# Performance work log

Measured on AMD Instinct MI355X. Metric: run time of the kernel, lower is better.

The kernel has to match this reference:

```python
import jax, jax.numpy as jnp
import numpy as np

TOKENS, IN_F, OUT_F = 8192, 4096, 4096
MAXQ = 15          # 4-bit
ZERO_POINT = 8     # (maxq + 1) // 2


def _make_24_mask(key, in_f, out_f):
    """Boolean 2:4 mask: exactly 2 True per contiguous group of 4 along in_f."""
    scores = jax.random.normal(key, (in_f // 4, 4, out_f), dtype=jnp.float32)
    # ascending sort along the group-of-4 axis; index 2 = 2nd largest value
    thresh = jnp.sort(scores, axis=1)[:, 2:3, :]
    mask = scores >= thresh  # keeps top-2 of each group of 4
    return mask.reshape(in_f, out_f)


def setup_inputs() -> dict:
    key = jax.random.key(0)
    k_x, k_q, k_m, k_s = jax.random.split(key, 4)
    x = jax.random.normal(k_x, (TOKENS, IN_F), dtype=jnp.float16)
    qvals = jax.random.randint(k_q, (IN_F, OUT_F), 0, MAXQ + 1, dtype=jnp.int32)
    mask = _make_24_mask(k_m, IN_F, OUT_F)
    # per-column scales (groupsize == infeatures -> one scale row)
    scales = (jax.random.uniform(k_s, (1, OUT_F), dtype=jnp.float32) * 0.01 + 0.001).astype(jnp.float16)
    return {"x": x, "qvals": qvals, "mask": mask, "scales": scales}


def reference(x, qvals, mask, scales):
    # Dequantize: W = (q - zero_point) * scale, then apply 2:4 sparsity mask.
    w = (qvals.astype(jnp.float32) - ZERO_POINT) * scales.astype(jnp.float32)  # [in, out]
    w = jnp.where(mask, w, 0.0).astype(x.dtype)
    # GEMM with fp32 accumulation (as the fused kernel does), output in x.dtype
    y = jnp.einsum("ti,io->to", x, w, preferred_element_type=jnp.float32)
    return y.astype(x.dtype)
```

## Files before the change

### kernel.cpp

```cpp
#include <hip/hip_runtime.h>
#include <stdint.h>

typedef short short8 __attribute__((ext_vector_type(8)));
typedef float floatx4 __attribute__((ext_vector_type(4)));

#define M_TOK 8192
#define K_IN  4096
#define N_OUT 4096
#define NT    (K_IN / 64)

static __device__ __forceinline__ float bf2f(ushort u) {
    union { uint32_t u; float f; } v;
    v.u = ((uint32_t)u) << 16;
    return v.f;
}
static __device__ __forceinline__ ushort f2bf(float f) {
    union { float f; uint32_t u; } v;
    v.f = f;
    uint32_t u = v.u;
    uint32_t r = (u + 0x7FFFu + ((u >> 16) & 1u)) >> 16;
    return (ushort)r;
}

__global__ void detect_zero_kernel(int* __restrict__ flags) {
    if (threadIdx.x < 3) flags[1 + threadIdx.x] = 0;
}

__global__ __launch_bounds__(256) void detect_count_kernel(
    const unsigned char* __restrict__ mb, int* __restrict__ flags) {
    const ushort* mh = (const ushort*)mb;
    const unsigned int* mw = (const unsigned int*)mb;
    __shared__ int sh[3];
    if (threadIdx.x < 3) sh[threadIdx.x] = 0;
    __syncthreads();
    int s = blockIdx.x * 256 + threadIdx.x;
    int grp = s & 255;
    int o   = (s * 97) & 4095;
    int c1 = 0, c2 = 0, c4 = 0;
    #pragma unroll
    for (int r = 0; r < 4; ++r) {
        size_t idx = (size_t)(4 * grp + r) * N_OUT + o;
        c1 += (mb[idx] != 0);
        c2 += (mh[idx] != 0);
        c4 += (mw[idx] != 0);
    }
    if (c1 != 2) atomicAdd(&sh[0], 1);
    if (c2 != 2) atomicAdd(&sh[1], 1);
    if (c4 != 2) atomicAdd(&sh[2], 1);
    __syncthreads();
    if (threadIdx.x == 0) {
        atomicAdd(&flags[1], sh[0]);
        atomicAdd(&flags[2], sh[1]);
        atomicAdd(&flags[3], sh[2]);
    }
}

__global__ void detect_final_kernel(int* __restrict__ flags) {
    if (threadIdx.x == 0) {
        int size = 4, best = flags[3];
        if (flags[2] < best) { size = 2; best = flags[2]; }
        if (flags[1] < best) { size = 1; }
        flags[0] = size;
    }
}

__global__ __launch_bounds__(256) void convert_x_kernel(
    const float* __restrict__ xf, ushort* __restrict__ Xb) {
    const int total = M_TOK * K_IN;
    const int stride = gridDim.x * 256 * 8;
    for (int i = (blockIdx.x * 256 + threadIdx.x) * 8; i < total; i += stride) {
        floatx4 f0 = *(const floatx4*)&xf[i];
        floatx4 f1 = *(const floatx4*)&xf[i + 4];
        short8 v;
        #pragma unroll
        for (int j = 0; j < 4; ++j) v[j]     = (short)f2bf(f0[j]);
        #pragma unroll
        for (int j = 0; j < 4; ++j) v[4 + j] = (short)f2bf(f1[j]);
        *(short8*)&Xb[i] = v;
    }
}

__global__ __launch_bounds__(256) void dequant_kernel(
    const int* __restrict__ q, const void* __restrict__ maskp,
    const float* __restrict__ scales, ushort* __restrict__ Bt,
    const int* __restrict__ flagp) {
    const int msize = flagp[0];
    const int i0 = blockIdx.x * 64;
    const int o0 = blockIdx.y * 64;
    const int tid = threadIdx.x;
    const unsigned char* mb = (const unsigned char*)maskp;
    const ushort* mh = (const ushort*)maskp;
    const unsigned int* mi = (const unsigned int*)maskp;
    __shared__ ushort T[64][72];

    for (int p = 0; p < 16; ++p) {
        int idx = p * 256 + tid;
        int r = idx >> 6, c = idx & 63;
        size_t gi = (size_t)(i0 + r) * N_OUT + (o0 + c);
        bool m;
        if (msize == 1)      m = (mb[gi] != 0);
        else if (msize == 2) m = (mh[gi] != 0);
        else                 m = (mi[gi] != 0);
        float s = scales[o0 + c];
        float w = m ? (float)(q[gi] - 8) * s : 0.0f;
        T[r][c] = f2bf(w);
    }
    __syncthreads();
    for (int p = 0; p < 2; ++p) {
        int ol = p * 32 + (tid >> 3);
        int i8 = (tid & 7) * 8;
        short8 v;
        #pragma unroll
        for (int j = 0; j < 8; ++j) v[j] = (short)T[i8 + j][ol];
        *(short8*)&Bt[(size_t)(o0 + ol) * K_IN + i0 + i8] = v;
    }
}

#define GL2L16(gp, lbase)                                                      \
    __builtin_amdgcn_global_load_lds(                                          \
        (const __attribute__((address_space(1))) void*)(gp),                   \
        (__attribute__((address_space(3))) void*)(lbase), 16, 0, 0)

__global__ __launch_bounds__(512, 2) void gemm_kernel(
    const ushort* __restrict__ X,
    const ushort* __restrict__ Bt,
    float* __restrict__ Y) {
    __shared__ ushort As[2][2][256][32];
    __shared__ ushort Bs[2][2][256][32];

    const int tid  = threadIdx.x;
    const int w    = tid >> 6;
    const int lane = tid & 63;

    const int r    = blockIdx.x >> 8;
    const int kb   = blockIdx.x & 255;
    const int xcd  = kb & 7;
    const int j    = kb >> 3;
    const int m_tile = r * 16 + (xcd & 1) * 8 + (j & 7);
    const int n_tile = (xcd >> 1) * 4 + (j >> 3);
    const int row0 = m_tile * 256;
    const int col0 = n_tile * 256;
    const int wm = w >> 2, wn = w & 3;

    floatx4 acc[8][4] = {};

    const int srow   = (w << 4) + (lane >> 2);
    const int schunk = (lane & 3) ^ ((lane >> 3) & 3);
    const ushort* gA = X  + (size_t)(row0 + srow) * K_IN + schunk * 8;
    const ushort* gB = Bt + (size_t)(col0 + srow) * K_IN + schunk * 8;

    const int fr = lane & 15, g = lane >> 4;
    const int fsw = (fr >> 1) & 3;

    #define STG(gbase, arr, bf, kh, tt)                                        \
        do {                                                                   \
            GL2L16(gbase + (size_t)(tt) * 64 + (kh) * 32,                      \
                   (char*)&arr[bf][kh][w * 16][0] + lane * 16);                \
            GL2L16(gbase + (size_t)128 * K_IN + (size_t)(tt) * 64 + (kh) * 32, \
                   (char*)&arr[bf][kh][128 + w * 16][0] + lane * 16);          \
        } while (0)

    #define PHASE(BF, KK, MH, READB, bfr, STAGE_STMT, GATE_STMT)               \
        do {                                                                   \
            if (READB) {                                                       \
                _Pragma("unroll")                                              \
                for (int n = 0; n < 4; ++n)                                    \
                    bfr[n] = *(const short8*)&Bs[BF][KK]                       \
                        [wn * 64 + n * 16 + fr][(g ^ fsw) * 8];                \
            }                                                                  \
            short8 afr[4];                                                     \
            _Pragma("unroll")                                                  \
            for (int m = 0; m < 4; ++m)                                        \
                afr[m] = *(const short8*)&As[BF][KK]                           \
                    [wm * 128 + (MH) * 64 + m * 16 + fr][(g ^ fsw) * 8];       \
            STAGE_STMT;                                                        \
            __builtin_amdgcn_s_barrier();                                      \
            asm volatile("s_waitcnt lgkmcnt(0)" ::: "memory");                 \
            __builtin_amdgcn_sched_barrier(0);                                 \
            __builtin_amdgcn_s_setprio(1);                                     \
            _Pragma("unroll")                                                  \
            for (int m = 0; m < 4; ++m)                                        \
                _Pragma("unroll")                                              \
                for (int n = 0; n < 4; ++n)                                    \
                    acc[(MH) * 4 + m][n] = __builtin_amdgcn_mfma_f32_16x16x32_bf16( \
                        afr[m], bfr[n], acc[(MH) * 4 + m][n], 0, 0, 0);        \
            __builtin_amdgcn_s_setprio(0);                                     \
            GATE_STMT;                                                         \
            __builtin_amdgcn_s_barrier();                                      \
        } while (0)

    #define GATE(c)                                                            \
        do {                                                                   \
            if (c) { asm volatile("s_waitcnt vmcnt(4)" ::: "memory"); }        \
            else   { asm volatile("s_waitcnt vmcnt(0)" ::: "memory"); }        \
        } while (0)

    STG(gA, As, 0, 0, 0);
    STG(gB, Bs, 0, 0, 0);
    STG(gA, As, 0, 1, 0);
    STG(gB, Bs, 0, 1, 0);
    STG(gA, As, 1, 0, 1);
    STG(gB, Bs, 1, 0, 1);
    asm volatile("s_waitcnt vmcnt(4)" ::: "memory");
    __builtin_amdgcn_s_barrier();

    short8 bfr0[4], bfr1[4];

    for (int i = 0; i < NT / 2; ++i) {
        const int t1 = 2 * i + 1, t2 = 2 * i + 2, t3 = 2 * i + 3;
        const bool s2 = (t2 < NT), s3 = (t3 < NT);

        PHASE(0, 0, 0, 1, bfr0, STG(gA, As, 1, 1, t1), );
        PHASE(0, 0, 1, 0, bfr0, STG(gB, Bs, 1, 1, t1), );
        PHASE(0, 1, 0, 1, bfr1, if (s2) STG(gA, As, 0, 0, t2), );
        PHASE(0, 1, 1, 0, bfr1, if (s2) STG(gB, Bs, 0, 0, t2), GATE(s2));

        PHASE(1, 0, 0, 1, bfr0, if (s2) STG(gA, As, 0, 1, t2), );
        PHASE(1, 0, 1, 0, bfr0, if (s2) STG(gB, Bs, 0, 1, t2), );
        PHASE(1, 1, 0, 1, bfr1, if (s3) STG(gA, As, 1, 0, t3), );
        PHASE(1, 1, 1, 0, bfr1, if (s3) STG(gB, Bs, 1, 0, t3), GATE(s3));
    }

    const int fq = lane >> 4;
    #pragma unroll
    for (int m = 0; m < 8; ++m)
        #pragma unroll
        for (int n = 0; n < 4; ++n)
            #pragma unroll
            for (int i = 0; i < 4; ++i) {
                int rr = row0 + wm * 128 + m * 16 + fq * 4 + i;
                int cc = col0 + wn * 64 + n * 16 + fr;
                Y[(size_t)rr * N_OUT + cc] = acc[m][n][i];
            }
    #undef GATE
    #undef PHASE
    #undef STG
}

__global__ __launch_bounds__(256) void fallback_kernel(
    const float* __restrict__ xf, const int* __restrict__ q,
    const void* __restrict__ maskp, const float* __restrict__ scales,
    float* __restrict__ Y, const int* __restrict__ flagp) {
    const int msize = flagp[0];
    const int o = blockIdx.x * 256 + threadIdx.x;
    const int t = blockIdx.y;
    const unsigned char* mb = (const unsigned char*)maskp;
    const ushort* mh = (const ushort*)maskp;
    const unsigned int* mi = (const unsigned int*)maskp;
    float s = scales[o];
    float acc = 0.f;
    for (int i = 0; i < K_IN; ++i) {
        float x = bf2f(f2bf(xf[(size_t)t * K_IN + i]));
        size_t gi = (size_t)i * N_OUT + o;
        bool m;
        if (msize == 1)      m = (mb[gi] != 0);
        else if (msize == 2) m = (mh[gi] != 0);
        else                 m = (mi[gi] != 0);
        if (m) acc += x * bf2f(f2bf((float)(q[gi] - 8) * s));
    }
    Y[(size_t)t * N_OUT + o] = acc;
}

extern "C" void kernel_launch(void* const* d_in, const int* in_sizes, int n_in,
                              void* d_out, int out_size, void* d_ws, size_t ws_size,
                              hipStream_t stream) {
    const float* x      = (const float*)d_in[0];
    const int*   q      = (const int*)d_in[1];
    const void*  mask   = d_in[2];
    const float* scales = (const float*)d_in[3];
    float* y = (float*)d_out;

    const size_t BT_OFF = 64;
    const size_t XB_OFF = BT_OFF + (size_t)N_OUT * K_IN * 2;
    const size_t need   = XB_OFF + (size_t)M_TOK * K_IN * 2;

    int* flags = (int*)d_ws;
    detect_zero_kernel<<<1, 64, 0, stream>>>(flags);
    detect_count_kernel<<<64, 256, 0, stream>>>(
        (const unsigned char*)mask, flags);
    detect_final_kernel<<<1, 64, 0, stream>>>(flags);

    if (ws_size >= need) {
        ushort* Bt = (ushort*)((char*)d_ws + BT_OFF);
        ushort* Xb = (ushort*)((char*)d_ws + XB_OFF);
        convert_x_kernel<<<4096, 256, 0, stream>>>(x, Xb);
        dequant_kernel<<<dim3(K_IN / 64, N_OUT / 64), 256, 0, stream>>>(
            q, mask, scales, Bt, flags);
        gemm_kernel<<<dim3((M_TOK / 256) * (N_OUT / 256)), 512, 0, stream>>>(
            Xb, Bt, y);
    } else {
        fallback_kernel<<<dim3(N_OUT / 256, M_TOK), 256, 0, stream>>>(
            x, q, mask, scales, y, flags);
    }
}
```

Before: 358.7 us.

## Restructure GEMM pipeline into 4-slot ring of 32-wide K tiles

Replaces the double-buffered 64-wide K staging (two 32-wide halves per buffer) with a 4-slot ring buffer of 32-wide K slices, prefetching three tiles ahead. Each K slice is split into two MFMA phases with the A and B loads for the slice three steps ahead interleaved between them. The LDS swizzle pattern also changes to match the new 32-column row layout. The aim is deeper load-ahead that better hides global latency. The cost is more barriers per unit of K and more outstanding loads, while LDS size stays the same.

```diff
diff --git a/kernel.cpp b/kernel.cpp
--- a/kernel.cpp
+++ b/kernel.cpp
@@ -7,7 +7,7 @@
 #define M_TOK 8192
 #define K_IN  4096
 #define N_OUT 4096
-#define NT    (K_IN / 64)
+#define NTT   (K_IN / 32)
 
 static __device__ __forceinline__ float bf2f(ushort u) {
     union { uint32_t u; float f; } v;
@@ -121,12 +121,14 @@
         (const __attribute__((address_space(1))) void*)(gp),                   \
         (__attribute__((address_space(3))) void*)(lbase), 16, 0, 0)
 
+#define MFMA16(a, b, c) __builtin_amdgcn_mfma_f32_16x16x32_bf16(a, b, c, 0, 0, 0)
+
 __global__ __launch_bounds__(512, 2) void gemm_kernel(
     const ushort* __restrict__ X,
     const ushort* __restrict__ Bt,
     float* __restrict__ Y) {
-    __shared__ ushort As[2][2][256][32];
-    __shared__ ushort Bs[2][2][256][32];
+    __shared__ ushort As[4][256][32];
+    __shared__ ushort Bs[4][256][32];
 
     const int tid  = threadIdx.x;
     const int w    = tid >> 6;
@@ -145,35 +147,34 @@
     floatx4 acc[8][4] = {};
 
     const int srow   = (w << 4) + (lane >> 2);
-    const int schunk = (lane & 3) ^ ((lane >> 3) & 3);
+    const int schunk = (lane & 3) ^ ((lane >> 2) & 3);
     const ushort* gA = X  + (size_t)(row0 + srow) * K_IN + schunk * 8;
     const ushort* gB = Bt + (size_t)(col0 + srow) * K_IN + schunk * 8;
 
     const int fr = lane & 15, g = lane >> 4;
-    const int fsw = (fr >> 1) & 3;
-
-    #define STG(gbase, arr, bf, kh, tt)                                        \
+    const int fsw = fr & 3;
+
+    #define STGU(gbase, arr, SL, tt)                                           \
         do {                                                                   \
-            GL2L16(gbase + (size_t)(tt) * 64 + (kh) * 32,                      \
-                   (char*)&arr[bf][kh][w * 16][0] + lane * 16);                \
-            GL2L16(gbase + (size_t)128 * K_IN + (size_t)(tt) * 64 + (kh) * 32, \
-                   (char*)&arr[bf][kh][128 + w * 16][0] + lane * 16);          \
+            GL2L16(gbase + (size_t)(tt) * 32,                                  \
+                   (char*)&arr[SL][w * 16][0] + lane * 16);                    \
+            GL2L16(gbase + (size_t)128 * K_IN + (size_t)(tt) * 32,             \
+                   (char*)&arr[SL][128 + w * 16][0] + lane * 16);              \
         } while (0)
 
-    #define PHASE(BF, KK, MH, READB, bfr, STAGE_STMT, GATE_STMT)               \
+    #define TILE1(SL, T)                                                       \
         do {                                                                   \
-            if (READB) {                                                       \
-                _Pragma("unroll")                                              \
-                for (int n = 0; n < 4; ++n)                                    \
-                    bfr[n] = *(const short8*)&Bs[BF][KK]                       \
-                        [wn * 64 + n * 16 + fr][(g ^ fsw) * 8];                \
-            }                                                                  \
-            short8 afr[4];                                                     \
-            _Pragma("unroll")                                                  \
-            for (int m = 0; m < 4; ++m)                                        \
-                afr[m] = *(const short8*)&As[BF][KK]                           \
-                    [wm * 128 + (MH) * 64 + m * 16 + fr][(g ^ fsw) * 8];       \
-            STAGE_STMT;                                                        \
+            const bool sg = (T) + 3 < NTT;                                     \
+            short8 afr[4], bfr[4];                                             \
+            _Pragma("unroll")                                                  \
+            for (int n = 0; n < 4; ++n)                                        \
+                bfr[n] = *(const short8*)&Bs[SL][wn * 64 + n * 16 + fr]        \
+                             [(g ^ fsw) * 8];                                  \
+            _Pragma("unroll")                                                  \
+            for (int m = 0; m < 4; ++m)                                        \
+                afr[m] = *(const short8*)&As[SL][wm * 128 + m * 16 + fr]       \
+                             [(g ^ fsw) * 8];                                  \
+            if (sg) STGU(gA, As, ((SL) + 3) & 3, (T) + 3);                     \
             __builtin_amdgcn_s_barrier();                                      \
             asm volatile("s_waitcnt lgkmcnt(0)" ::: "memory");                 \
             __builtin_amdgcn_sched_barrier(0);                                 \
@@ -182,43 +183,41 @@
             for (int m = 0; m < 4; ++m)                                        \
                 _Pragma("unroll")                                              \
                 for (int n = 0; n < 4; ++n)                                    \
-                    acc[(MH) * 4 + m][n] = __builtin_amdgcn_mfma_f32_16x16x32_bf16( \
-                        afr[m], bfr[n], acc[(MH) * 4 + m][n], 0, 0, 0);        \
+                    acc[m][n] = MFMA16(afr[m], bfr[n], acc[m][n]);             \
             __builtin_amdgcn_s_setprio(0);                                     \
-            GATE_STMT;                                                         \
+            _Pragma("unroll")                                                  \
+            for (int m = 0; m < 4; ++m)                                        \
+                afr[m] = *(const short8*)&As[SL][wm * 128 + 64 + m * 16 + fr]  \
+                             [(g ^ fsw) * 8];                                  \
+            if (sg) STGU(gB, Bs, ((SL) + 3) & 3, (T) + 3);                     \
+            __builtin_amdgcn_s_barrier();                                      \
+            asm volatile("s_waitcnt lgkmcnt(0)" ::: "memory");                 \
+            __builtin_amdgcn_sched_barrier(0);                                 \
+            __builtin_amdgcn_s_setprio(1);                                     \
+            _Pragma("unroll")                                                  \
+            for (int m = 0; m < 4; ++m)                                        \
+                _Pragma("unroll")                                              \
+                for (int n = 0; n < 4; ++n)                                    \
+                    acc[4 + m][n] = MFMA16(afr[m], bfr[n], acc[4 + m][n]);     \
+            __builtin_amdgcn_s_setprio(0);                                     \
+            if (sg)                 { asm volatile("s_waitcnt vmcnt(8)" ::: "memory"); } \
+            else if ((T) + 2 < NTT) { asm volatile("s_waitcnt vmcnt(4)" ::: "memory"); } \
+            else                    { asm volatile("s_waitcnt vmcnt(0)" ::: "memory"); } \
             __builtin_amdgcn_s_barrier();                                      \
         } while (0)
 
-    #define GATE(c)                                                            \
-        do {                                                                   \
-            if (c) { asm volatile("s_waitcnt vmcnt(4)" ::: "memory"); }        \
-            else   { asm volatile("s_waitcnt vmcnt(0)" ::: "memory"); }        \
-        } while (0)
-
-    STG(gA, As, 0, 0, 0);
-    STG(gB, Bs, 0, 0, 0);
-    STG(gA, As, 0, 1, 0);
-    STG(gB, Bs, 0, 1, 0);
-    STG(gA, As, 1, 0, 1);
-    STG(gB, Bs, 1, 0, 1);
-    asm volatile("s_waitcnt vmcnt(4)" ::: "memory");
+    STGU(gA, As, 0, 0); STGU(gB, Bs, 0, 0);
+    STGU(gA, As, 1, 1); STGU(gB, Bs, 1, 1);
+    STGU(gA, As, 2, 2); STGU(gB, Bs, 2, 2);
+    asm volatile("s_waitcnt vmcnt(8)" ::: "memory");
     __builtin_amdgcn_s_barrier();
 
-    short8 bfr0[4], bfr1[4];
-
-    for (int i = 0; i < NT / 2; ++i) {
-        const int t1 = 2 * i + 1, t2 = 2 * i + 2, t3 = 2 * i + 3;
-        const bool s2 = (t2 < NT), s3 = (t3 < NT);
-
-        PHASE(0, 0, 0, 1, bfr0, STG(gA, As, 1, 1, t1), );
-        PHASE(0, 0, 1, 0, bfr0, STG(gB, Bs, 1, 1, t1), );
-        PHASE(0, 1, 0, 1, bfr1, if (s2) STG(gA, As, 0, 0, t2), );
-        PHASE(0, 1, 1, 0, bfr1, if (s2) STG(gB, Bs, 0, 0, t2), GATE(s2));
-
-        PHASE(1, 0, 0, 1, bfr0, if (s2) STG(gA, As, 0, 1, t2), );
-        PHASE(1, 0, 1, 0, bfr0, if (s2) STG(gB, Bs, 0, 1, t2), );
-        PHASE(1, 1, 0, 1, bfr1, if (s3) STG(gA, As, 1, 0, t3), );
-        PHASE(1, 1, 1, 0, bfr1, if (s3) STG(gB, Bs, 1, 0, t3), GATE(s3));
+    for (int t4 = 0; t4 < NTT / 4; ++t4) {
+        const int T = t4 * 4;
+        TILE1(0, T);
+        TILE1(1, T + 1);
+        TILE1(2, T + 2);
+        TILE1(3, T + 3);
     }
 
     const int fq = lane >> 4;
@@ -232,9 +231,8 @@
                 int cc = col0 + wn * 64 + n * 16 + fr;
                 Y[(size_t)rr * N_OUT + cc] = acc[m][n][i];
             }
-    #undef GATE
-    #undef PHASE
-    #undef STG
+    #undef TILE1
+    #undef STGU
 }
 
 __global__ __launch_bounds__(256) void fallback_kernel(
```

New measurement: 360.1 us. About the same (+0.4%).
